# Kernel optimization log

Hardware: AMD Instinct MI355X
Metric: run time of the kernel (lower is better)

The kernel has to match this reference:

```python
import jax, jax.numpy as jnp
import numpy as np

NUM_HEADS = 8
AGENT_NUM = 144
POOL_SIZE = 12  # int(sqrt(agent_num))


def _adaptive_pool_matrix(H, out):
    # Row i averages input rows [floor(i*H/out), ceil((i+1)*H/out)) -- PyTorch AdaptiveAvgPool2d semantics.
    P = np.zeros((out, H), dtype=np.float32)
    for i in range(out):
        s = (i * H) // out
        e = -((-(i + 1) * H) // out)
        P[i, s:e] = 1.0 / (e - s)
    return jnp.asarray(P)


def setup_inputs() -> dict:
    key = jax.random.key(0)
    ks = jax.random.split(key, 4)
    b, n, c = 16, 3136, 512
    return {
        "x": jax.random.normal(ks[0], (b, n, c), dtype=jnp.float32),
        "qkv_w": jax.random.normal(ks[1], (3 * c, c), dtype=jnp.float32) * 0.02,
        "proj_w": jax.random.normal(ks[2], (c, c), dtype=jnp.float32) * 0.02,
        "proj_b": jnp.zeros((c,), dtype=jnp.float32),
        "dwc_w": jax.random.normal(ks[3], (c, 1, 3, 3), dtype=jnp.float32) * 0.1,
        "dwc_b": jnp.zeros((c,), dtype=jnp.float32),
    }


def reference(x, qkv_w, proj_w, proj_b, dwc_w, dwc_b):
    b, n, c = x.shape
    H = NUM_HEADS
    d = c // H
    hh = int(n ** 0.5)  # 56
    scale = d ** -0.5

    qkv = x @ qkv_w.T  # (b, n, 3c)
    q, k, v = jnp.split(qkv, 3, axis=-1)

    # adaptive avg pool of q (as b,h,w,c image) down to 12x12 -> agent tokens
    P = _adaptive_pool_matrix(hh, POOL_SIZE)  # (12, 56)
    agent = jnp.einsum('ph,qw,bhwc->bpqc', P, P, q.reshape(b, hh, hh, c))
    agent = agent.reshape(b, AGENT_NUM, c)

    def heads(t):
        return t.reshape(b, -1, H, d).transpose(0, 2, 1, 3)  # (b, H, L, d)

    qh, kh, vh, ah = heads(q), heads(k), heads(v), heads(agent)

    # stage 1: agent-to-key attention
    agent_attn = jax.nn.softmax((ah * scale) @ kh.transpose(0, 1, 3, 2), axis=-1)  # (b,H,144,n)
    agent_v = agent_attn @ vh  # (b,H,144,d)

    # stage 2: query-to-agent attention
    q_attn = jax.nn.softmax((qh * scale) @ ah.transpose(0, 1, 3, 2), axis=-1)  # (b,H,n,144)
    out = (q_attn @ agent_v).transpose(0, 2, 1, 3).reshape(b, n, c)

    # depthwise 3x3 conv residual on v image
    v_img = v.reshape(b, hh, hh, c).transpose(0, 3, 1, 2)  # NCHW
    dw = jax.lax.conv_general_dilated(
        v_img, dwc_w, window_strides=(1, 1), padding='SAME',
        feature_group_count=c, dimension_numbers=('NCHW', 'OIHW', 'NCHW'))
    dw = dw + dwc_b[None, :, None, None]
    out = out + dw.transpose(0, 2, 3, 1).reshape(b, n, c)

    return out @ proj_w.T + proj_b
```

## Files before the change

kernel.cpp:

```cpp
#include <hip/hip_runtime.h>
#include <hip/hip_bf16.h>
#include <math.h>

typedef unsigned short u16;
typedef __attribute__((ext_vector_type(8))) unsigned short u16x8;
typedef __attribute__((ext_vector_type(8))) short bf16x8;
typedef __attribute__((ext_vector_type(4))) float f32x4;

#define BATCH 16
#define NTOK  3136
#define CHN   512
#define NH    8
#define HD    64
#define HHW   56
#define NAG   144
#define PS    12

#define S1PP   72
#define S2PP   168

__device__ __forceinline__ float b2f(u16 u) {
    unsigned int x = ((unsigned int)u) << 16;
    float f;
    __builtin_memcpy(&f, &x, 4);
    return f;
}
__device__ __forceinline__ u16 f2b(float f) {
    unsigned int x;
    __builtin_memcpy(&x, &f, 4);
    unsigned int lsb = (x >> 16) & 1u;
    x += 0x7fffu + lsb;
    return (u16)(x >> 16);
}
__device__ __forceinline__ void store1(float* p, float v) { *p = v; }
__device__ __forceinline__ void store1(u16* p, float v)   { *p = f2b(v); }

__global__ __launch_bounds__(256) void cvt_f32_bf16_kernel(
    const float* __restrict__ src, u16* __restrict__ dst, int n4)
{
    const int idx = blockIdx.x * 256 + threadIdx.x;
    if (idx >= n4) return;
    float4 v = reinterpret_cast<const float4*>(src)[idx];
    ushort4 o;
    o.x = f2b(v.x); o.y = f2b(v.y); o.z = f2b(v.z); o.w = f2b(v.w);
    reinterpret_cast<ushort4*>(dst)[idx] = o;
}

template <typename OT, bool BIAS>
__global__ __launch_bounds__(256) void mfma_gemm_kernel(
    const u16* __restrict__ A, const u16* __restrict__ W,
    const float* __restrict__ bias, OT* __restrict__ out)
{
    __shared__ u16 Asm[128 * 64];
    __shared__ u16 Bsm[128 * 64];

    const int tid  = threadIdx.x;
    const int lane = tid & 63;
    const int w    = tid >> 6;
    const int m0   = blockIdx.x * 128;
    const int n0   = blockIdx.y * 128;
    const int wm   = (w & 1) * 64;
    const int wn   = (w >> 1) * 64;

    const int srow = lane >> 3;
    const int scol = (lane & 7) * 8;

    f32x4 acc[4][4] = {};

    for (int kt = 0; kt < 8; ++kt) {
        const int k0 = kt * 64;
        __syncthreads();
        #pragma unroll
        for (int i = 0; i < 4; ++i) {
            const int rb = w * 8 + i * 32;
            __builtin_amdgcn_global_load_lds(
                (const __attribute__((address_space(1))) void*)
                    (A + (size_t)(m0 + rb + srow) * 512 + k0 + scol),
                (__attribute__((address_space(3))) void*)(Asm + rb * 64),
                16, 0, 0);
        }
        #pragma unroll
        for (int i = 0; i < 4; ++i) {
            const int rb = w * 8 + i * 32;
            __builtin_amdgcn_global_load_lds(
                (const __attribute__((address_space(1))) void*)
                    (W + (size_t)(n0 + rb + srow) * 512 + k0 + scol),
                (__attribute__((address_space(3))) void*)(Bsm + rb * 64),
                16, 0, 0);
        }
        __syncthreads();

        #pragma unroll
        for (int kh = 0; kh < 2; ++kh) {
            bf16x8 af[4], bfr[4];
            #pragma unroll
            for (int t = 0; t < 4; ++t)
                af[t] = *reinterpret_cast<const bf16x8*>(
                    &Asm[(wm + t * 16 + (lane & 15)) * 64 + kh * 32 + (lane >> 4) * 8]);
            #pragma unroll
            for (int t = 0; t < 4; ++t)
                bfr[t] = *reinterpret_cast<const bf16x8*>(
                    &Bsm[(wn + t * 16 + (lane & 15)) * 64 + kh * 32 + (lane >> 4) * 8]);
            #pragma unroll
            for (int i = 0; i < 4; ++i)
                #pragma unroll
                for (int j = 0; j < 4; ++j)
                    acc[i][j] = __builtin_amdgcn_mfma_f32_16x16x32_bf16(
                        af[i], bfr[j], acc[i][j], 0, 0, 0);
        }
    }

    const int quad = lane >> 4;
    const int col  = lane & 15;
    #pragma unroll
    for (int j = 0; j < 4; ++j) {
        const int n = n0 + wn + j * 16 + col;
        const float bv = BIAS ? bias[n] : 0.f;
        #pragma unroll
        for (int i = 0; i < 4; ++i) {
            #pragma unroll
            for (int r = 0; r < 4; ++r) {
                const int m = m0 + wm + i * 16 + quad * 4 + r;
                store1(&out[(size_t)m * 512 + n], acc[i][j][r] + bv);
            }
        }
    }
}

__global__ __launch_bounds__(256) void pool_x_kernel(
    const float* __restrict__ x, u16* __restrict__ x_pool)
{
    const int b = blockIdx.x, pq = blockIdx.y;
    const int p = pq / PS, qq = pq % PS;
    const int sp_ = (p * HHW) / PS, ep_ = ((p + 1) * HHW + PS - 1) / PS;
    const int sq_ = (qq * HHW) / PS, eq_ = ((qq + 1) * HHW + PS - 1) / PS;
    const float inv = 1.0f / (float)((ep_ - sp_) * (eq_ - sq_));
    for (int ch = threadIdx.x; ch < CHN; ch += 256) {
        float acc = 0.f;
        for (int y = sp_; y < ep_; ++y)
            for (int xx = sq_; xx < eq_; ++xx)
                acc += x[((size_t)b * NTOK + y * HHW + xx) * CHN + ch];
        x_pool[((size_t)b * NAG + pq) * CHN + ch] = f2b(acc * inv);
    }
}

__global__ __launch_bounds__(256) void transpose_v_kernel(
    const u16* __restrict__ v, u16* __restrict__ vt)
{
    __shared__ u16 T[64 * S1PP + 32];
    const int t0 = blockIdx.x * 64;
    const int c0 = blockIdx.y * 64;
    const int b  = blockIdx.z;

    const int r  = threadIdx.x >> 2;
    const int cc = (threadIdx.x & 3) * 16;
    const u16* src = v + ((size_t)b * NTOK + t0 + r) * CHN + c0 + cc;
    u16x8 a0 = *reinterpret_cast<const u16x8*>(src);
    u16x8 a1 = *reinterpret_cast<const u16x8*>(src + 8);
    const int skw = (cc >> 4) * 8;
    #pragma unroll
    for (int j = 0; j < 8; ++j) T[(cc + j) * S1PP + r + skw] = a0[j];
    #pragma unroll
    for (int j = 0; j < 8; ++j) T[(cc + 8 + j) * S1PP + r + skw] = a1[j];
    __syncthreads();

    const int cr  = threadIdx.x >> 2;
    const int tt  = (threadIdx.x & 3) * 16;
    const int rsk = (cr >> 4) * 8;
    u16* dst = vt + ((size_t)b * CHN + c0 + cr) * NTOK + t0 + tt;
    *reinterpret_cast<u16x8*>(dst)     = *reinterpret_cast<const u16x8*>(&T[cr * S1PP + tt + rsk]);
    *reinterpret_cast<u16x8*>(dst + 8) = *reinterpret_cast<const u16x8*>(&T[cr * S1PP + tt + 8 + rsk]);
}

__global__ __launch_bounds__(64) void stage1_mfma_kernel(
    const u16* __restrict__ k, const u16* __restrict__ vt,
    const u16* __restrict__ agent, u16* __restrict__ avt)
{
    __shared__ u16 Pl[16 * S1PP];

    const int lb   = blockIdx.x;
    const int work = (lb & 7) * 144 + (lb >> 3);
    const int at   = work % 9;
    const int r2   = work / 9;
    const int h    = r2 & 7;
    const int b    = r2 >> 3;

    const int lane = threadIdx.x;
    const int c = lane & 15, g = lane >> 4;

    const u16* kp = k  + (size_t)b * NTOK * CHN + h * HD;
    const u16* vp = vt + ((size_t)(b * NH + h)) * HD * NTOK;
    const u16* ap = agent + ((size_t)b * NAG + at * 16 + c) * CHN + h * HD + g * 8;

    bf16x8 af0 = *reinterpret_cast<const bf16x8*>(ap);
    bf16x8 af1 = *reinterpret_cast<const bf16x8*>(ap + 32);

    f32x4 accO[4] = {};
    float m_ = -1e30f, l_ = 0.f;

    bf16x8 kf[8];
    #pragma unroll
    for (int kt = 0; kt < 4; ++kt)
        #pragma unroll
        for (int ks = 0; ks < 2; ++ks)
            kf[kt * 2 + ks] = *reinterpret_cast<const bf16x8*>(
                kp + (size_t)(kt * 16 + c) * CHN + ks * 32 + g * 8);

    for (int key0 = 0; key0 < NTOK; key0 += 64) {
        bf16x8 vf[8];
        #pragma unroll
        for (int dt = 0; dt < 4; ++dt)
            #pragma unroll
            for (int kk = 0; kk < 2; ++kk)
                vf[dt * 2 + kk] = *reinterpret_cast<const bf16x8*>(
                    vp + (size_t)(dt * 16 + c) * NTOK + key0 + kk * 32 + g * 8);
        bf16x8 kn[8];
        const bool more = (key0 + 64) < NTOK;
        if (more) {
            #pragma unroll
            for (int kt = 0; kt < 4; ++kt)
                #pragma unroll
                for (int ks = 0; ks < 2; ++ks)
                    kn[kt * 2 + ks] = *reinterpret_cast<const bf16x8*>(
                        kp + (size_t)(key0 + 64 + kt * 16 + c) * CHN + ks * 32 + g * 8);
        }

        f32x4 s[4] = {};
        #pragma unroll
        for (int kt = 0; kt < 4; ++kt) {
            s[kt] = __builtin_amdgcn_mfma_f32_16x16x32_bf16(kf[kt * 2 + 0], af0, s[kt], 0, 0, 0);
            s[kt] = __builtin_amdgcn_mfma_f32_16x16x32_bf16(kf[kt * 2 + 1], af1, s[kt], 0, 0, 0);
        }

        float tmax = -1e30f;
        #pragma unroll
        for (int kt = 0; kt < 4; ++kt)
            #pragma unroll
            for (int r = 0; r < 4; ++r) tmax = fmaxf(tmax, s[kt][r]);
        tmax = fmaxf(tmax, __shfl_xor(tmax, 16));
        tmax = fmaxf(tmax, __shfl_xor(tmax, 32));

        const float mnew  = fmaxf(m_, tmax * 0.125f);
        const float alpha = __expf(m_ - mnew);
        float psum = 0.f;
        #pragma unroll
        for (int kt = 0; kt < 4; ++kt) {
            float p0 = __expf(s[kt][0] * 0.125f - mnew);
            float p1 = __expf(s[kt][1] * 0.125f - mnew);
            float p2 = __expf(s[kt][2] * 0.125f - mnew);
            float p3 = __expf(s[kt][3] * 0.125f - mnew);
            psum += (p0 + p1) + (p2 + p3);
            ushort4 pk;
            pk.x = f2b(p0); pk.y = f2b(p1); pk.z = f2b(p2); pk.w = f2b(p3);
            *reinterpret_cast<ushort4*>(&Pl[c * S1PP + kt * 16 + g * 4]) = pk;
        }
        psum += __shfl_xor(psum, 16);
        psum += __shfl_xor(psum, 32);
        l_ = l_ * alpha + psum;
        m_ = mnew;
        #pragma unroll
        for (int dt = 0; dt < 4; ++dt) {
            accO[dt][0] *= alpha; accO[dt][1] *= alpha;
            accO[dt][2] *= alpha; accO[dt][3] *= alpha;
        }

        asm volatile("s_waitcnt lgkmcnt(0)" ::: "memory");
        __builtin_amdgcn_sched_barrier(0);

        bf16x8 pf0 = *reinterpret_cast<const bf16x8*>(&Pl[c * S1PP + g * 8]);
        bf16x8 pf1 = *reinterpret_cast<const bf16x8*>(&Pl[c * S1PP + 32 + g * 8]);

        #pragma unroll
        for (int dt = 0; dt < 4; ++dt) {
            accO[dt] = __builtin_amdgcn_mfma_f32_16x16x32_bf16(vf[dt * 2 + 0], pf0, accO[dt], 0, 0, 0);
            accO[dt] = __builtin_amdgcn_mfma_f32_16x16x32_bf16(vf[dt * 2 + 1], pf1, accO[dt], 0, 0, 0);
        }

        if (more) {
            #pragma unroll
            for (int i = 0; i < 8; ++i) kf[i] = kn[i];
        }
    }

    const float invl = 1.f / l_;
    const size_t dbase = (size_t)(b * NH + h) * HD;
    #pragma unroll
    for (int dt = 0; dt < 4; ++dt)
        #pragma unroll
        for (int r = 0; r < 4; ++r)
            avt[(dbase + dt * 16 + g * 4 + r) * NAG + at * 16 + c] =
                f2b(accO[dt][r] * invl);
}

__global__ __launch_bounds__(256, 3) void stage2_mfma_kernel(
    const u16* __restrict__ q,
    const u16* __restrict__ agent,
    const u16* __restrict__ avt,
    const u16* __restrict__ v,
    const float* __restrict__ dwc_w,
    const float* __restrict__ dwc_b,
    u16* __restrict__ xattn)
{
    __shared__ u16 Pl[4 * 16 * S2PP];
    __shared__ float dwW[HD * 9];
    __shared__ float dwB[HD];

    const int h   = blockIdx.y;
    const int b   = blockIdx.z;
    const int tid = threadIdx.x;
    const int w    = tid >> 6;
    const int lane = tid & 63;
    const int c = lane & 15, g = lane >> 4;
    const int q0 = (blockIdx.x * 4 + w) * 16;
    const int qg = q0 + c;
    const int y = qg / HHW, xx = qg % HHW;

    ushort4 vtap[9][4];
    unsigned vmask = 0;
    const u16* vq = v + ((size_t)b * NTOK + qg) * CHN + h * HD + g * 4;
    #pragma unroll
    for (int dy = -1; dy <= 1; ++dy) {
        #pragma unroll
        for (int dx = -1; dx <= 1; ++dx) {
            const int tap = (dy + 1) * 3 + (dx + 1);
            const int yy = y + dy, xc = xx + dx;
            const bool ok = (yy >= 0 && yy < HHW && xc >= 0 && xc < HHW);
            if (ok) vmask |= 1u << tap;
            const u16* vr = vq + (ok ? (ptrdiff_t)(dy * HHW + dx) * CHN : 0);
            #pragma unroll
            for (int dt = 0; dt < 4; ++dt)
                vtap[tap][dt] = *reinterpret_cast<const ushort4*>(vr + dt * 16);
        }
    }

    const u16* qp = q + ((size_t)b * NTOK + qg) * CHN + h * HD + g * 8;
    bf16x8 qf0 = *reinterpret_cast<const bf16x8*>(qp);
    bf16x8 qf1 = *reinterpret_cast<const bf16x8*>(qp + 32);

    for (int idx = tid; idx < HD * 9; idx += 256)
        dwW[idx] = dwc_w[(h * HD + idx / 9) * 9 + (idx % 9)];
    if (tid < HD) dwB[tid] = dwc_b[h * HD + tid];
    __syncthreads();

    u16* Pw = &Pl[w * 16 * S2PP];

    f32x4 s[9] = {};
    const u16* ap = agent + ((size_t)b * NAG + c) * CHN + h * HD + g * 8;
    #pragma unroll
    for (int t = 0; t < 9; ++t) {
        bf16x8 af0 = *reinterpret_cast<const bf16x8*>(ap + (size_t)t * 16 * CHN);
        bf16x8 af1 = *reinterpret_cast<const bf16x8*>(ap + (size_t)t * 16 * CHN + 32);
        s[t] = __builtin_amdgcn_mfma_f32_16x16x32_bf16(af0, qf0, s[t], 0, 0, 0);
        s[t] = __builtin_amdgcn_mfma_f32_16x16x32_bf16(af1, qf1, s[t], 0, 0, 0);
    }

    float mx = -1e30f;
    #pragma unroll
    for (int t = 0; t < 9; ++t)
        #pragma unroll
        for (int r = 0; r < 4; ++r) mx = fmaxf(mx, s[t][r]);
    mx = fmaxf(mx, __shfl_xor(mx, 16));
    mx = fmaxf(mx, __shfl_xor(mx, 32));
    mx *= 0.125f;

    float ls = 0.f;
    #pragma unroll
    for (int t = 0; t < 9; ++t) {
        float p0 = __expf(s[t][0] * 0.125f - mx);
        float p1 = __expf(s[t][1] * 0.125f - mx);
        float p2 = __expf(s[t][2] * 0.125f - mx);
        float p3 = __expf(s[t][3] * 0.125f - mx);
        ls += (p0 + p1) + (p2 + p3);
        ushort4 pk;
        pk.x = f2b(p0); pk.y = f2b(p1); pk.z = f2b(p2); pk.w = f2b(p3);
        *reinterpret_cast<ushort4*>(&Pw[c * S2PP + t * 16 + g * 4]) = pk;
    }
    ls += __shfl_xor(ls, 16);
    ls += __shfl_xor(ls, 32);
    const float inv = 1.f / ls;

    asm volatile("s_waitcnt lgkmcnt(0)" ::: "memory");
    __builtin_amdgcn_sched_barrier(0);

    f32x4 o[4] = {};
    const u16* avp = avt + (size_t)(b * NH + h) * HD * NAG;
    #pragma unroll
    for (int sl = 0; sl < 4; ++sl) {
        bf16x8 pf = *reinterpret_cast<const bf16x8*>(&Pw[c * S2PP + sl * 32 + g * 8]);
        #pragma unroll
        for (int dt = 0; dt < 4; ++dt) {
            bf16x8 avf = *reinterpret_cast<const bf16x8*>(
                avp + (size_t)(dt * 16 + c) * NAG + sl * 32 + g * 8);
            o[dt] = __builtin_amdgcn_mfma_f32_16x16x32_bf16(avf, pf, o[dt], 0, 0, 0);
        }
    }
    {
        bf16x8 pf = {};
        bf16x8 avf[4] = {{0,0,0,0,0,0,0,0},{0,0,0,0,0,0,0,0},
                         {0,0,0,0,0,0,0,0},{0,0,0,0,0,0,0,0}};
        if (g < 2) {
            pf = *reinterpret_cast<const bf16x8*>(&Pw[c * S2PP + 128 + g * 8]);
            #pragma unroll
            for (int dt = 0; dt < 4; ++dt)
                avf[dt] = *reinterpret_cast<const bf16x8*>(
                    avp + (size_t)(dt * 16 + c) * NAG + 128 + g * 8);
        }
        #pragma unroll
        for (int dt = 0; dt < 4; ++dt)
            o[dt] = __builtin_amdgcn_mfma_f32_16x16x32_bf16(avf[dt], pf, o[dt], 0, 0, 0);
    }

    float res[4][4];
    #pragma unroll
    for (int dt = 0; dt < 4; ++dt)
        #pragma unroll
        for (int r = 0; r < 4; ++r)
            res[dt][r] = o[dt][r] * inv + dwB[dt * 16 + g * 4 + r];

    #pragma unroll
    for (int tap = 0; tap < 9; ++tap) {
        if (vmask & (1u << tap)) {
            #pragma unroll
            for (int dt = 0; dt < 4; ++dt) {
                const ushort4 vv = vtap[tap][dt];
                res[dt][0] += b2f(vv.x) * dwW[(dt * 16 + g * 4 + 0) * 9 + tap];
                res[dt][1] += b2f(vv.y) * dwW[(dt * 16 + g * 4 + 1) * 9 + tap];
                res[dt][2] += b2f(vv.z) * dwW[(dt * 16 + g * 4 + 2) * 9 + tap];
                res[dt][3] += b2f(vv.w) * dwW[(dt * 16 + g * 4 + 3) * 9 + tap];
            }
        }
    }

    u16* outp = xattn + ((size_t)b * NTOK + qg) * CHN + h * HD + g * 4;
    #pragma unroll
    for (int dt = 0; dt < 4; ++dt) {
        ushort4 o4;
        o4.x = f2b(res[dt][0]); o4.y = f2b(res[dt][1]);
        o4.z = f2b(res[dt][2]); o4.w = f2b(res[dt][3]);
        *reinterpret_cast<ushort4*>(outp + dt * 16) = o4;
    }
}

extern "C" void kernel_launch(void* const* d_in, const int* in_sizes, int n_in,
                              void* d_out, int out_size, void* d_ws, size_t ws_size,
                              hipStream_t stream)
{
    const float* x      = (const float*)d_in[0];
    const float* qkv_w  = (const float*)d_in[1];
    const float* proj_w = (const float*)d_in[2];
    const float* proj_b = (const float*)d_in[3];
    const float* dwc_w  = (const float*)d_in[4];
    const float* dwc_b  = (const float*)d_in[5];
    float* out = (float*)d_out;

    const size_t nqkv = (size_t)BATCH * NTOK * CHN;
    u16* xb  = (u16*)d_out;
    u16* vt  = xb + nqkv;
    u16* qb  = xb + nqkv;
    u16* kb  = (u16*)d_in[0];
    u16* vb  = kb + nqkv;
    u16* attn = kb;

    char* p = (char*)d_ws;
    u16* x_pool  = (u16*)p;  p += (size_t)BATCH * NAG * CHN * 2;
    u16* agent   = (u16*)p;  p += (size_t)BATCH * NAG * CHN * 2;
    u16* avt     = (u16*)p;  p += (size_t)BATCH * NH * HD * NAG * 2;
    u16* wb      = (u16*)p;
    u16* Wq_b = wb;
    u16* Wk_b = wb + (size_t)262144;
    u16* Wv_b = wb + (size_t)524288;
    u16* Wp_b = wb + (size_t)786432;

    pool_x_kernel<<<dim3(BATCH, NAG), 256, 0, stream>>>(x, x_pool);
    cvt_f32_bf16_kernel<<<(int)(nqkv / 4 + 255) / 256, 256, 0, stream>>>(x, xb, (int)(nqkv / 4));
    cvt_f32_bf16_kernel<<<(786432 / 4 + 255) / 256, 256, 0, stream>>>(qkv_w, wb, 786432 / 4);
    cvt_f32_bf16_kernel<<<(262144 / 4 + 255) / 256, 256, 0, stream>>>(proj_w, Wp_b, 262144 / 4);
    mfma_gemm_kernel<u16, false><<<dim3(18, 4), 256, 0, stream>>>(x_pool, Wq_b, nullptr, agent);
    mfma_gemm_kernel<u16, false><<<dim3(392, 4), 256, 0, stream>>>(xb, Wk_b, nullptr, kb);
    mfma_gemm_kernel<u16, false><<<dim3(392, 4), 256, 0, stream>>>(xb, Wv_b, nullptr, vb);
    transpose_v_kernel<<<dim3(NTOK / 64, CHN / 64, BATCH), 256, 0, stream>>>(vb, vt);
    stage1_mfma_kernel<<<dim3(1152), 64, 0, stream>>>(kb, vt, agent, avt);
    mfma_gemm_kernel<u16, false><<<dim3(392, 4), 256, 0, stream>>>(xb, Wq_b, nullptr, qb);
    stage2_mfma_kernel<<<dim3(49, NH, BATCH), 256, 0, stream>>>(
        qb, agent, avt, vb, dwc_w, dwc_b, attn);
    mfma_gemm_kernel<float, true><<<dim3(392, 4), 256, 0, stream>>>(attn, Wp_b, proj_b, out);
}
```

Baseline: 795.8 us.

## Stage agent and agent_v tiles in LDS and fold depthwise conv early

The stage-2 kernel now cooperatively loads each block's agent tile and transposed agent_v tile into padded shared memory, so the MFMA loops read operands from LDS instead of from global memory in every wave. The depthwise 3x3 conv is accumulated right after the v loads into 16 floats, rather than keeping 36 ushort4 tap registers live across the attention math. This lowers register pressure, which allows raising the launch bound from 3 to 4 blocks per SM. The cost is roughly 40KB of extra LDS per block, which may itself limit occupancy, plus an additional load phase before the barrier.

```diff
diff --git a/kernel.cpp b/kernel.cpp
--- a/kernel.cpp
+++ b/kernel.cpp
@@ -17,7 +17,9 @@
 #define PS    12
 
 #define S1PP   72
-#define S2PP   168
+#define S2PP   152
+#define ASP    72
+#define AVP    152
 
 __device__ __forceinline__ float b2f(u16 u) {
     unsigned int x = ((unsigned int)u) << 16;
@@ -292,7 +294,7 @@
                 f2b(accO[dt][r] * invl);
 }
 
-__global__ __launch_bounds__(256, 3) void stage2_mfma_kernel(
+__global__ __launch_bounds__(256, 4) void stage2_mfma_kernel(
     const u16* __restrict__ q,
     const u16* __restrict__ agent,
     const u16* __restrict__ avt,
@@ -301,7 +303,9 @@
     const float* __restrict__ dwc_b,
     u16* __restrict__ xattn)
 {
-    __shared__ u16 Pl[4 * 16 * S2PP];
+    __shared__ __align__(16) u16 As[NAG * ASP];
+    __shared__ __align__(16) u16 AVs[HD * AVP];
+    __shared__ __align__(16) u16 Pl[4 * 16 * S2PP];
     __shared__ float dwW[HD * 9];
     __shared__ float dwB[HD];
 
@@ -315,41 +319,80 @@
     const int qg = q0 + c;
     const int y = qg / HHW, xx = qg % HHW;
 
-    ushort4 vtap[9][4];
-    unsigned vmask = 0;
-    const u16* vq = v + ((size_t)b * NTOK + qg) * CHN + h * HD + g * 4;
-    #pragma unroll
-    for (int dy = -1; dy <= 1; ++dy) {
-        #pragma unroll
-        for (int dx = -1; dx <= 1; ++dx) {
-            const int tap = (dy + 1) * 3 + (dx + 1);
-            const int yy = y + dy, xc = xx + dx;
-            const bool ok = (yy >= 0 && yy < HHW && xc >= 0 && xc < HHW);
-            if (ok) vmask |= 1u << tap;
-            const u16* vr = vq + (ok ? (ptrdiff_t)(dy * HHW + dx) * CHN : 0);
-            #pragma unroll
-            for (int dt = 0; dt < 4; ++dt)
-                vtap[tap][dt] = *reinterpret_cast<const ushort4*>(vr + dt * 16);
-        }
-    }
-
     const u16* qp = q + ((size_t)b * NTOK + qg) * CHN + h * HD + g * 8;
     bf16x8 qf0 = *reinterpret_cast<const bf16x8*>(qp);
     bf16x8 qf1 = *reinterpret_cast<const bf16x8*>(qp + 32);
 
-    for (int idx = tid; idx < HD * 9; idx += 256)
-        dwW[idx] = dwc_w[(h * HD + idx / 9) * 9 + (idx % 9)];
-    if (tid < HD) dwB[tid] = dwc_b[h * HD + tid];
+    {
+        const u16* ab = agent + (size_t)b * NAG * CHN + h * HD;
+        for (int idx = tid; idx < NAG * 4; idx += 256) {
+            const int r = idx >> 2, cc = (idx & 3) * 16;
+            *reinterpret_cast<u16x8*>(&As[r * ASP + cc]) =
+                *reinterpret_cast<const u16x8*>(ab + (size_t)r * CHN + cc);
+            *reinterpret_cast<u16x8*>(&As[r * ASP + cc + 8]) =
+                *reinterpret_cast<const u16x8*>(ab + (size_t)r * CHN + cc + 8);
+        }
+        const u16* avb = avt + (size_t)(b * NH + h) * HD * NAG;
+        for (int idx = tid; idx < HD * 18; idx += 256) {
+            const int r = idx / 18, cc = (idx % 18) * 8;
+            *reinterpret_cast<u16x8*>(&AVs[r * AVP + cc]) =
+                *reinterpret_cast<const u16x8*>(avb + (size_t)r * NAG + cc);
+        }
+        for (int idx = tid; idx < HD * 9; idx += 256)
+            dwW[idx] = dwc_w[(h * HD + idx / 9) * 9 + (idx % 9)];
+        if (tid < HD) dwB[tid] = dwc_b[h * HD + tid];
+    }
     __syncthreads();
 
+    float conv[4][4];
+    #pragma unroll
+    for (int dt = 0; dt < 4; ++dt)
+        #pragma unroll
+        for (int r = 0; r < 4; ++r) conv[dt][r] = 0.f;
+    {
+        const u16* vq = v + ((size_t)b * NTOK + qg) * CHN + h * HD + g * 4;
+        #pragma unroll
+        for (int dy = -1; dy <= 1; ++dy) {
+            #pragma unroll
+            for (int dx = -1; dx <= 1; ++dx) {
+                const int tap = (dy + 1) * 3 + (dx + 1);
+                const int yy = y + dy, xc = xx + dx;
+                const bool ok = (yy >= 0 && yy < HHW && xc >= 0 && xc < HHW);
+                const u16* vr = vq + (ok ? (ptrdiff_t)(dy * HHW + dx) * CHN : 0);
+                ushort4 vv0 = *reinterpret_cast<const ushort4*>(vr);
+                ushort4 vv1 = *reinterpret_cast<const ushort4*>(vr + 16);
+                ushort4 vv2 = *reinterpret_cast<const ushort4*>(vr + 32);
+                ushort4 vv3 = *reinterpret_cast<const ushort4*>(vr + 48);
+                if (ok) {
+                    const float* wt = &dwW[(g * 4) * 9 + tap];
+                    conv[0][0] += b2f(vv0.x) * wt[(0 * 16 + 0) * 9];
+                    conv[0][1] += b2f(vv0.y) * wt[(0 * 16 + 1) * 9];
+                    conv[0][2] += b2f(vv0.z) * wt[(0 * 16 + 2) * 9];
+                    conv[0][3] += b2f(vv0.w) * wt[(0 * 16 + 3) * 9];
+                    conv[1][0] += b2f(vv1.x) * wt[(1 * 16 + 0) * 9];
+                    conv[1][1] += b2f(vv1.y) * wt[(1 * 16 + 1) * 9];
+                    conv[1][2] += b2f(vv1.z) * wt[(1 * 16 + 2) * 9];
+                    conv[1][3] += b2f(vv1.w) * wt[(1 * 16 + 3) * 9];
+                    conv[2][0] += b2f(vv2.x) * wt[(2 * 16 + 0) * 9];
+                    conv[2][1] += b2f(vv2.y) * wt[(2 * 16 + 1) * 9];
+                    conv[2][2] += b2f(vv2.z) * wt[(2 * 16 + 2) * 9];
+                    conv[2][3] += b2f(vv2.w) * wt[(2 * 16 + 3) * 9];
+                    conv[3][0] += b2f(vv3.x) * wt[(3 * 16 + 0) * 9];
+                    conv[3][1] += b2f(vv3.y) * wt[(3 * 16 + 1) * 9];
+                    conv[3][2] += b2f(vv3.z) * wt[(3 * 16 + 2) * 9];
+                    conv[3][3] += b2f(vv3.w) * wt[(3 * 16 + 3) * 9];
+                }
+            }
+        }
+    }
+
     u16* Pw = &Pl[w * 16 * S2PP];
 
     f32x4 s[9] = {};
-    const u16* ap = agent + ((size_t)b * NAG + c) * CHN + h * HD + g * 8;
     #pragma unroll
     for (int t = 0; t < 9; ++t) {
-        bf16x8 af0 = *reinterpret_cast<const bf16x8*>(ap + (size_t)t * 16 * CHN);
-        bf16x8 af1 = *reinterpret_cast<const bf16x8*>(ap + (size_t)t * 16 * CHN + 32);
+        bf16x8 af0 = *reinterpret_cast<const bf16x8*>(&As[(t * 16 + c) * ASP + g * 8]);
+        bf16x8 af1 = *reinterpret_cast<const bf16x8*>(&As[(t * 16 + c) * ASP + 32 + g * 8]);
         s[t] = __builtin_amdgcn_mfma_f32_16x16x32_bf16(af0, qf0, s[t], 0, 0, 0);
         s[t] = __builtin_amdgcn_mfma_f32_16x16x32_bf16(af1, qf1, s[t], 0, 0, 0);
     }
@@ -383,14 +426,13 @@
     __builtin_amdgcn_sched_barrier(0);
 
     f32x4 o[4] = {};
-    const u16* avp = avt + (size_t)(b * NH + h) * HD * NAG;
     #pragma unroll
     for (int sl = 0; sl < 4; ++sl) {
         bf16x8 pf = *reinterpret_cast<const bf16x8*>(&Pw[c * S2PP + sl * 32 + g * 8]);
         #pragma unroll
         for (int dt = 0; dt < 4; ++dt) {
             bf16x8 avf = *reinterpret_cast<const bf16x8*>(
-                avp + (size_t)(dt * 16 + c) * NAG + sl * 32 + g * 8);
+                &AVs[(dt * 16 + c) * AVP + sl * 32 + g * 8]);
             o[dt] = __builtin_amdgcn_mfma_f32_16x16x32_bf16(avf, pf, o[dt], 0, 0, 0);
         }
     }
@@ -403,40 +445,21 @@
             #pragma unroll
             for (int dt = 0; dt < 4; ++dt)
                 avf[dt] = *reinterpret_cast<const bf16x8*>(
-                    avp + (size_t)(dt * 16 + c) * NAG + 128 + g * 8);
+                    &AVs[(dt * 16 + c) * AVP + 128 + g * 8]);
         }
         #pragma unroll
         for (int dt = 0; dt < 4; ++dt)
             o[dt] = __builtin_amdgcn_mfma_f32_16x16x32_bf16(avf[dt], pf, o[dt], 0, 0, 0);
     }
 
-    float res[4][4];
-    #pragma unroll
-    for (int dt = 0; dt < 4; ++dt)
-        #pragma unroll
-        for (int r = 0; r < 4; ++r)
-            res[dt][r] = o[dt][r] * inv + dwB[dt * 16 + g * 4 + r];
-
-    #pragma unroll
-    for (int tap = 0; tap < 9; ++tap) {
-        if (vmask & (1u << tap)) {
-            #pragma unroll
-            for (int dt = 0; dt < 4; ++dt) {
-                const ushort4 vv = vtap[tap][dt];
-                res[dt][0] += b2f(vv.x) * dwW[(dt * 16 + g * 4 + 0) * 9 + tap];
-                res[dt][1] += b2f(vv.y) * dwW[(dt * 16 + g * 4 + 1) * 9 + tap];
-                res[dt][2] += b2f(vv.z) * dwW[(dt * 16 + g * 4 + 2) * 9 + tap];
-                res[dt][3] += b2f(vv.w) * dwW[(dt * 16 + g * 4 + 3) * 9 + tap];
-            }
-        }
-    }
-
     u16* outp = xattn + ((size_t)b * NTOK + qg) * CHN + h * HD + g * 4;
     #pragma unroll
     for (int dt = 0; dt < 4; ++dt) {
         ushort4 o4;
-        o4.x = f2b(res[dt][0]); o4.y = f2b(res[dt][1]);
-        o4.z = f2b(res[dt][2]); o4.w = f2b(res[dt][3]);
+        o4.x = f2b(o[dt][0] * inv + dwB[dt * 16 + g * 4 + 0] + conv[dt][0]);
+        o4.y = f2b(o[dt][1] * inv + dwB[dt * 16 + g * 4 + 1] + conv[dt][1]);
+        o4.z = f2b(o[dt][2] * inv + dwB[dt * 16 + g * 4 + 2] + conv[dt][2]);
+        o4.w = f2b(o[dt][3] * inv + dwB[dt * 16 + g * 4 + 3] + conv[dt][3]);
         *reinterpret_cast<ushort4*>(outp + dt * 16) = o4;
     }
 }
```

New measurement: 739.4 us. 7.1% less time.
